# Kernel optimization log

Measured on AMD Instinct MI355X. Metric: run time of the kernel, lower is better.

Reference implementation:

```python
import jax, jax.numpy as jnp
import numpy as np

B, C, OC, H, W = 2, 64, 128, 96, 96
HD, DI, N, R, K = C // 2, C, 16, 2, 4  # VSSBlock: hidden=C/2, d_inner=2*hidden=C, d_state, dt_rank, 4 scan dirs
EPS = 1e-5


def _conv(x, w, b, pad, groups=1):
    y = jax.lax.conv_general_dilated(x, w, (1, 1), pad, feature_group_count=groups,
                                     dimension_numbers=('NCHW', 'OIHW', 'NCHW'))
    return y + b[None, :, None, None]


def _ln(x, w, b):
    m = x.mean(-1, keepdims=True)
    v = x.var(-1, keepdims=True)
    return (x - m) * jax.lax.rsqrt(v + EPS) * w + b


def _selective_scan(xs, dts, Bs, Cs, A, D):
    # xs, dts: (B,K,DI,L); Bs, Cs: (B,K,N,L); A: (K,DI,N); D: (K,DI)
    dts = jax.nn.softplus(dts)

    def step(h, inp):
        u_t, dt_t, B_t, C_t = inp
        dA = jnp.exp(dt_t[..., None] * A)                         # (B,K,DI,N)
        h = dA * h + (dt_t * u_t)[..., None] * B_t[:, :, None, :]
        return h, jnp.einsum('bkdn,bkn->bkd', h, C_t)

    seq = (jnp.moveaxis(xs, -1, 0), jnp.moveaxis(dts, -1, 0),
           jnp.moveaxis(Bs, -1, 0), jnp.moveaxis(Cs, -1, 0))
    h0 = jnp.zeros(xs.shape[:3] + (A.shape[-1],), xs.dtype)
    _, ys = jax.lax.scan(step, h0, seq)
    return jnp.moveaxis(ys, 0, -1) + D[None, :, :, None] * xs


def _vss_block(x, ln_w, ln_b, in_w, conv_w, conv_b, xproj_w, dtproj_w, dtproj_b,
               A_logs, Ds, on_w, on_b, out_w):
    # x: (B,H,W,HD); VMamba SS2D with 4-direction cross-scan + residual
    b, hh, ww, _ = x.shape
    L = hh * ww
    h = _ln(x, ln_w, ln_b)
    xz = h @ in_w                                   # (B,H,W,2*DI)
    xp, z = jnp.split(xz, 2, axis=-1)
    xc = jnp.transpose(xp, (0, 3, 1, 2))            # (B,DI,H,W)
    xc = jax.nn.silu(_conv(xc, conv_w, conv_b, ((1, 1), (1, 1)), groups=DI))
    x_flat = xc.reshape(b, DI, L)
    x_wh = jnp.transpose(xc, (0, 1, 3, 2)).reshape(b, DI, L)
    x2 = jnp.stack([x_flat, x_wh], axis=1)
    xs = jnp.concatenate([x2, jnp.flip(x2, -1)], axis=1)      # (B,4,DI,L)
    x_dbl = jnp.einsum('bkdl,kcd->bkcl', xs, xproj_w)
    dts, Bs, Cs = jnp.split(x_dbl, [R, R + N], axis=2)
    dts = jnp.einsum('bkrl,kdr->bkdl', dts, dtproj_w) + dtproj_b[None, :, :, None]
    A = -jnp.exp(A_logs)
    ys = _selective_scan(xs, dts, Bs, Cs, A, Ds)              # (B,4,DI,L)
    inv = jnp.flip(ys[:, 2:4], -1)
    unwh = lambda t: jnp.transpose(t.reshape(b, DI, ww, hh), (0, 1, 3, 2)).reshape(b, DI, L)
    y = ys[:, 0] + inv[:, 0] + unwh(ys[:, 1]) + unwh(inv[:, 1])
    y = jnp.transpose(y.reshape(b, DI, hh, ww), (0, 2, 3, 1))
    y = _ln(y, on_w, on_b) * jax.nn.silu(z)
    return x + y @ out_w


def _forward(x, ms_dw33_w, ms_dw33_b, ms_in_w, ms_in_b, ms_scale,
             vss_ln_w, vss_ln_b, vss_in_w, vss_conv_w, vss_conv_b, vss_xproj_w,
             vss_dtproj_w, vss_dtproj_b, vss_A_logs, vss_Ds, vss_on_w, vss_on_b, vss_out_w,
             ma_conv_w, ma_conv_b, adw_h_w, adw_h_b, adw_w_w, adw_w_b,
             pw_w, pw_b, bn_w, bn_b, bn_mean, bn_var):
    vss = (vss_ln_w, vss_ln_b, vss_in_w, vss_conv_w, vss_conv_b, vss_xproj_w,
           vss_dtproj_w, vss_dtproj_b, vss_A_logs, vss_Ds, vss_on_w, vss_on_b, vss_out_w)
    # --- MambaSplit (shared VSSBlock applied to both channel halves) ---
    xd = _conv(x, ms_dw33_w, ms_dw33_b, ((1, 1), (1, 1)), groups=C)
    x1, x2 = jnp.split(xd, 2, axis=1)

    def branch(xp):
        y = _vss_block(jnp.transpose(xp, (0, 2, 3, 1)), *vss)
        return ms_scale * xp + jnp.transpose(y, (0, 3, 1, 2))

    xm = jnp.concatenate([branch(x1), branch(x2)], axis=1)
    m = xm.mean((2, 3), keepdims=True)
    v = xm.var((2, 3), keepdims=True)
    xm = (xm - m) * jax.lax.rsqrt(v + EPS) * ms_in_w[None, :, None, None] + ms_in_b[None, :, None, None]
    xm = jax.nn.leaky_relu(xm, 0.01)
    # --- MaxAvg (global avg+max pool -> 3x3 conv on 1x1 map -> sigmoid gate) ---
    pooled = jnp.concatenate([x.mean((2, 3), keepdims=True), x.max((2, 3), keepdims=True)], axis=1)
    gate = jax.nn.sigmoid(_conv(pooled, ma_conv_w, ma_conv_b, ((1, 1), (1, 1))))
    xs_ = xm + gate * x
    # --- AxialDW ---
    xs_ = xs_ + _conv(xs_, adw_h_w, adw_h_b, ((1, 1), (0, 0)), groups=C) \
              + _conv(xs_, adw_w_w, adw_w_b, ((0, 0), (1, 1)), groups=C)
    # --- BN (eval) + ReLU, 1x1 conv, 2x2 maxpool ---
    skip = jax.nn.relu((xs_ - bn_mean[None, :, None, None]) * jax.lax.rsqrt(bn_var[None, :, None, None] + EPS)
                       * bn_w[None, :, None, None] + bn_b[None, :, None, None])
    out = _conv(skip, pw_w, pw_b, ((0, 0), (0, 0)))
    down = jax.lax.reduce_window(out, -jnp.inf, jax.lax.max, (1, 1, 2, 2), (1, 1, 2, 2), 'VALID')
    return down, skip


def setup_inputs() -> dict:
    key = jax.random.key(0)
    ks = jax.random.split(key, 16)
    r = lambda i, shape, s=0.02: jax.random.normal(ks[i], shape, jnp.float32) * s
    return {
        'x': jax.random.normal(ks[0], (B, C, H, W), jnp.float32),
        'ms_dw33_w': r(1, (C, 1, 3, 3), 0.1), 'ms_dw33_b': jnp.zeros(C),
        'ms_in_w': jnp.ones(C), 'ms_in_b': jnp.zeros(C),
        'ms_scale': jnp.ones((1,)),
        'vss_ln_w': jnp.ones(HD), 'vss_ln_b': jnp.zeros(HD),
        'vss_in_w': r(2, (HD, 2 * DI)),
        'vss_conv_w': r(3, (DI, 1, 3, 3), 0.1), 'vss_conv_b': jnp.zeros(DI),
        'vss_xproj_w': r(4, (K, R + 2 * N, DI)),
        'vss_dtproj_w': r(5, (K, DI, R), 0.1), 'vss_dtproj_b': r(6, (K, DI), 0.1),
        'vss_A_logs': jnp.tile(jnp.log(jnp.arange(1, N + 1, dtype=jnp.float32)), (K, DI, 1)),
        'vss_Ds': jnp.ones((K, DI)),
        'vss_on_w': jnp.ones(DI), 'vss_on_b': jnp.zeros(DI),
        'vss_out_w': r(7, (DI, HD)),
        'ma_conv_w': r(8, (C, 2 * C, 3, 3), 0.05), 'ma_conv_b': jnp.zeros(C),
        'adw_h_w': r(9, (C, 1, 3, 1), 0.1), 'adw_h_b': jnp.zeros(C),
        'adw_w_w': r(10, (C, 1, 1, 3), 0.1), 'adw_w_b': jnp.zeros(C),
        'pw_w': r(11, (OC, C, 1, 1)), 'pw_b': jnp.zeros(OC),
        'bn_w': jnp.ones(C), 'bn_b': jnp.zeros(C),
        'bn_mean': jnp.zeros(C), 'bn_var': jnp.ones(C),
    }


def reference(x, ms_dw33_w, ms_dw33_b, ms_in_w, ms_in_b, ms_scale,
              vss_ln_w, vss_ln_b, vss_in_w, vss_conv_w, vss_conv_b, vss_xproj_w,
              vss_dtproj_w, vss_dtproj_b, vss_A_logs, vss_Ds, vss_on_w, vss_on_b, vss_out_w,
              ma_conv_w, ma_conv_b, adw_h_w, adw_h_b, adw_w_w, adw_w_b,
              pw_w, pw_b, bn_w, bn_b, bn_mean, bn_var):
    return _forward(x, ms_dw33_w, ms_dw33_b, ms_in_w, ms_in_b, ms_scale,
                    vss_ln_w, vss_ln_b, vss_in_w, vss_conv_w, vss_conv_b, vss_xproj_w,
                    vss_dtproj_w, vss_dtproj_b, vss_A_logs, vss_Ds, vss_on_w, vss_on_b, vss_out_w,
                    ma_conv_w, ma_conv_b, adw_h_w, adw_h_b, adw_w_w, adw_w_b,
                    pw_w, pw_b, bn_w, bn_b, bn_mean, bn_var)
```

## Files before the change

kernel.cpp:

```cpp
#include <hip/hip_runtime.h>
#include <hip/hip_bf16.h>

typedef __hip_bfloat16 bf16;
#define DEV __device__ __forceinline__

constexpr int B_ = 2, C_ = 64, H_ = 96, W_ = 96, L_ = 9216;
constexpr int HD_ = 32, DI_ = 64, N_ = 16, K_ = 4, BB_ = 4;
constexpr int OC_ = 128;
constexpr int CH_ = 384, CL_ = 24;
constexpr int SEGN = 32, SEGC = 12;
constexpr int BROW = 20;
constexpr float EPSF = 1e-5f;
constexpr int DOWN_SZ = B_ * OC_ * 48 * 48;

typedef __attribute__((ext_vector_type(8))) short short8;
typedef __attribute__((ext_vector_type(4))) float f32x4;
typedef __attribute__((ext_vector_type(2))) float f32x2;

DEV float softplusf(float x) { return x > 15.f ? x : __logf(1.f + __expf(x)); }
DEV float b2f(bf16 v) { return __bfloat162float(v); }
DEV float lo16f(unsigned v) { return __uint_as_float(v << 16); }
DEV float hi16f(unsigned v) { return __uint_as_float(v & 0xffff0000u); }
DEV f32x2 pk2(unsigned w) { f32x2 r = {lo16f(w), hi16f(w)}; return r; }
DEV f32x2 lo2(f32x4 q) { f32x2 r = {q.x, q.y}; return r; }
DEV f32x2 hi2(f32x4 q) { f32x2 r = {q.z, q.w}; return r; }
DEV unsigned pkbf(float a, float b) {
  __hip_bfloat162 t;
  t.x = __float2bfloat16(a);
  t.y = __float2bfloat16(b);
  return *reinterpret_cast<unsigned*>(&t);
}
DEV void unpk8(uint4 a, float* v) {
  v[0] = lo16f(a.x); v[1] = hi16f(a.x); v[2] = lo16f(a.y); v[3] = hi16f(a.y);
  v[4] = lo16f(a.z); v[5] = hi16f(a.z); v[6] = lo16f(a.w); v[7] = hi16f(a.w);
}
DEV void unpk(uint4 a, uint4 b, float* v) {
  unpk8(a, v); unpk8(b, v + 8);
}

__constant__ float kLogN[16] = {
  0.0f, 0.69314718f, 1.09861229f, 1.38629436f, 1.60943791f, 1.79175947f,
  1.94591015f, 2.07944154f, 2.19722458f, 2.30258509f, 2.39789527f,
  2.48490665f, 2.56494936f, 2.63905733f, 2.70805020f, 2.77258872f};

DEV void pow_tree2(float e1, f32x2* ep) {
  float e2 = e1 * e1;
  ep[0].x = e1; ep[0].y = e2;
  f32x2 b2v = {e2, e2};
  ep[1] = ep[0] * b2v;
  float e4 = ep[1].y;
  f32x2 b4v = {e4, e4};
  ep[2] = ep[0] * b4v;
  ep[3] = ep[1] * b4v;
  float e8 = ep[3].y;
  f32x2 b8v = {e8, e8};
  ep[4] = ep[0] * b8v;
  ep[5] = ep[1] * b8v;
  ep[6] = ep[2] * b8v;
  ep[7] = ep[3] * b8v;
}

__global__ __launch_bounds__(256, 4) void k_front(
    const float* __restrict__ x, const float* __restrict__ dw33w,
    const float* __restrict__ dw33b, const float* __restrict__ lnw,
    const float* __restrict__ lnb, const float* __restrict__ inw,
    const float* __restrict__ xpw, const float* __restrict__ alog,
    float* __restrict__ xd, bf16* __restrict__ xzAh, bf16* __restrict__ xzBh,
    bf16* __restrict__ wh, float* __restrict__ aux) {
  int bb = blockIdx.y, t = threadIdx.x;
  int b = bb & 1, co = (bb >> 1) * HD_;
  int idx0 = blockIdx.x * 32;
  if (bb == 0) {
    int i = blockIdx.x * 256 + t;
    if (i < 144 * 64) {
      int n = i >> 6;
      wh[i] = __float2bfloat16(n < 136 ? xpw[i] : 0.f);
    }
    if (blockIdx.x == 0) {
      int kd = t;
      const float* al = alog + kd * N_;
      float a0 = al[0];
      bool lin = true;
#pragma unroll
      for (int n = 1; n < N_; n++) lin = lin && (fabsf(al[n] - a0 - kLogN[n]) < 3e-5f);
      aux[kd] = -__expf(a0);
      aux[256 + kd] = lin ? 1.f : 0.f;
#pragma unroll
      for (int n = 0; n < N_; n++) aux[512 + kd * N_ + n] = -__expf(al[n]);
    }
  }
  __shared__ float xds[32 * 36];
  __shared__ float meanA[32], rstdA[32];
  for (int i = t; i < 1024; i += 256) {
    int cl = i >> 5, ii = i & 31;
    int sp = idx0 + ii, wi = sp % 96, hi = sp / 96;
    int cg = b * C_ + co + cl;
    float acc = dw33b[co + cl];
#pragma unroll
    for (int dy = -1; dy <= 1; dy++) {
      int hh = hi + dy; if (hh < 0 || hh >= H_) continue;
#pragma unroll
      for (int dx = -1; dx <= 1; dx++) {
        int ww = wi + dx; if (ww < 0 || ww >= W_) continue;
        acc = fmaf(x[(size_t)cg * L_ + sp + dy * 96 + dx],
                   dw33w[(co + cl) * 9 + (dy + 1) * 3 + (dx + 1)], acc);
      }
    }
    xds[cl * 36 + ii] = acc;
    xd[(size_t)cg * L_ + sp] = acc;
  }
  __syncthreads();
  if (t < 32) {
    float s = 0.f, sq = 0.f;
#pragma unroll
    for (int c = 0; c < 32; c++) { float v = xds[c * 36 + t]; s += v; sq = fmaf(v, v, sq); }
    float mean = s * (1.f / HD_);
    float var = sq * (1.f / HD_) - mean * mean;
    meanA[t] = mean; rstdA[t] = rsqrtf(var + EPSF);
  }
  __syncthreads();
  for (int i = t; i < 1024; i += 256) {
    int c = i >> 5, idx = i & 31;
    float v = xds[c * 36 + idx];
    xds[c * 36 + idx] = (v - meanA[idx]) * rstdA[idx] * lnw[c] + lnb[c];
  }
  __syncthreads();
  int oc = t & 127, g = t >> 7;
  float acc[16];
#pragma unroll
  for (int j = 0; j < 16; j++) acc[j] = 0.f;
  for (int c = 0; c < 32; c++) {
    float wv = inw[c * 128 + oc];
    const float4* row = reinterpret_cast<const float4*>(&xds[c * 36 + g * 16]);
#pragma unroll
    for (int j4 = 0; j4 < 4; j4++) {
      float4 xv = row[j4];
      acc[j4 * 4 + 0] = fmaf(xv.x, wv, acc[j4 * 4 + 0]);
      acc[j4 * 4 + 1] = fmaf(xv.y, wv, acc[j4 * 4 + 1]);
      acc[j4 * 4 + 2] = fmaf(xv.z, wv, acc[j4 * 4 + 2]);
      acc[j4 * 4 + 3] = fmaf(xv.w, wv, acc[j4 * 4 + 3]);
    }
  }
  int occ = oc & 63;
  if (oc < 64) {
#pragma unroll
    for (int j = 0; j < 16; j++)
      xzAh[(size_t)(bb * L_ + idx0 + g * 16 + j) * 64 + occ] = __float2bfloat16(acc[j]);
  } else {
#pragma unroll
    for (int j = 0; j < 16; j++)
      xzBh[(size_t)(bb * L_ + idx0 + g * 16 + j) * 64 + occ] = __float2bfloat16(acc[j]);
  }
}

__global__ void k_dwsilu(const bf16* __restrict__ xzAh, const float* __restrict__ cw,
                         const float* __restrict__ cb, bf16* __restrict__ xch,
                         bf16* __restrict__ xcht) {
  int t = blockIdx.x * 256 + threadIdx.x;
  int dp = t & 31, rp = t >> 5;
  int bb = blockIdx.y;
  int d0 = dp * 2;
  int wi = rp % 96, hp = rp / 96;
  int hi0 = hp * 2;
  const unsigned* src = (const unsigned*)xzAh;
  float a00 = cb[d0], a01 = cb[d0 + 1];
  float a10 = a00, a11 = a01;
#pragma unroll
  for (int r4 = 0; r4 < 4; r4++) {
    int rr = hi0 - 1 + r4;
    if (rr < 0 || rr >= H_) continue;
#pragma unroll
    for (int c3 = 0; c3 < 3; c3++) {
      int cc = wi - 1 + c3;
      if (cc < 0 || cc >= W_) continue;
      unsigned v = src[(size_t)(bb * L_ + rr * 96 + cc) * 32 + dp];
      float vl = lo16f(v), vh = hi16f(v);
      if (r4 <= 2) {
        a00 = fmaf(vl, cw[d0 * 9 + r4 * 3 + c3], a00);
        a01 = fmaf(vh, cw[(d0 + 1) * 9 + r4 * 3 + c3], a01);
      }
      if (r4 >= 1) {
        a10 = fmaf(vl, cw[d0 * 9 + (r4 - 1) * 3 + c3], a10);
        a11 = fmaf(vh, cw[(d0 + 1) * 9 + (r4 - 1) * 3 + c3], a11);
      }
    }
  }
  a00 = a00 / (1.f + __expf(-a00));
  a01 = a01 / (1.f + __expf(-a01));
  a10 = a10 / (1.f + __expf(-a10));
  a11 = a11 / (1.f + __expf(-a11));
  unsigned o0 = pkbf(a00, a01), o1 = pkbf(a10, a11);
  int idx0 = hi0 * 96 + wi;
  ((unsigned*)xch)[((size_t)bb * L_ + idx0) * 32 + dp] = o0;
  ((unsigned*)xch)[((size_t)bb * L_ + idx0 + 96) * 32 + dp] = o1;
  int it0 = wi * 96 + hi0;
  ((unsigned*)xcht)[((size_t)bb * L_ + it0) * 32 + dp] = o0;
  ((unsigned*)xcht)[((size_t)bb * L_ + it0 + 1) * 32 + dp] = o1;
}

__global__ __launch_bounds__(256, 4) void k_xdbl_mfma(
    const bf16* __restrict__ xch, const bf16* __restrict__ wh,
    float* __restrict__ xdblB, float* __restrict__ xdblC) {
  int w = threadIdx.x >> 6, lane = threadIdx.x & 63;
  int bb = blockIdx.y;
  int mtile = blockIdx.x * 4 + w;
  int idx0 = mtile * 16;
  int m = lane & 15, quad = lane >> 4;
  const bf16* arow = xch + ((size_t)bb * L_ + idx0 + m) * 64 + quad * 8;
  short8 a0 = *reinterpret_cast<const short8*>(arow);
  short8 a1 = *reinterpret_cast<const short8*>(arow + 32);
  int ntb = blockIdx.z * 3;
#pragma unroll
  for (int it = 0; it < 3; it++) {
    int nt = ntb + it;
    int n = nt * 16 + m;
    const bf16* brow = wh + n * 64 + quad * 8;
    short8 b0 = *reinterpret_cast<const short8*>(brow);
    short8 b1 = *reinterpret_cast<const short8*>(brow + 32);
    f32x4 acc = {0.f, 0.f, 0.f, 0.f};
    acc = __builtin_amdgcn_mfma_f32_16x16x32_bf16(a0, b0, acc, 0, 0, 0);
    acc = __builtin_amdgcn_mfma_f32_16x16x32_bf16(a1, b1, acc, 0, 0, 0);
    if (n < 136) {
      int k4 = (n >= 102) ? 3 : (n >= 68) ? 2 : (n >= 34) ? 1 : 0;
      int c = n - k4 * 34;
#pragma unroll
      for (int i = 0; i < 4; i++) {
        int r = idx0 + quad * 4 + i;
        int hi2 = r / 96, wi2 = r - hi2 * 96;
        int tr = wi2 * 96 + hi2;
        int ls = (k4 == 0) ? r : (k4 == 1) ? tr : (k4 == 2) ? (L_ - 1 - r) : (L_ - 1 - tr);
        size_t row = (size_t)(bb * K_ + k4) * L_ + ls;
        if (c < 2)       xdblB[row * BROW + 16 + c] = acc[i];
        else if (c < 18) xdblB[row * BROW + (c - 2)] = acc[i];
        else             xdblC[row * 16 + (c - 18)] = acc[i];
      }
    }
  }
}

__global__ __launch_bounds__(256, 4) void k_scan1(
    const float* __restrict__ xdblB, const bf16* __restrict__ xch,
    const bf16* __restrict__ xcht, const float* __restrict__ dtw,
    const float* __restrict__ dtb, const float* __restrict__ aux,
    bf16* __restrict__ hbuf, float* __restrict__ ssum) {
  int w = threadIdx.x >> 6, d = threadIdx.x & 63;
  int bx = blockIdx.x;
  int chunk = bx * 4 + w, k = blockIdx.y, bb = blockIdx.z;
  const float* bB = xdblB + (size_t)(bb * K_ + k) * L_ * BROW;
  __shared__ __align__(16) float sB[96 * BROW];
  {
    const uint4* src = (const uint4*)(bB + (size_t)bx * 96 * BROW);
    uint4* dst = (uint4*)sB;
    for (int i = threadIdx.x; i < 480; i += 256) dst[i] = src[i];
  }
  __syncthreads();
  float w0 = dtw[(k * DI_ + d) * 2 + 0], w1 = dtw[(k * DI_ + d) * 2 + 1];
  float bia = dtb[k * DI_ + d];
  float A1 = aux[k * 64 + d];
  bool chain = (__ballot(aux[256 + k * 64 + d] > 0.5f) == ~0ull);
  const bf16* ub = ((k & 1) ? xcht : xch) + (size_t)bb * L_ * DI_;
  int ls0 = chunk * CL_;
  int uidx0 = (k & 2) ? (L_ - 1 - ls0) : ls0;
  int ustep = (k & 2) ? -1 : 1;
  float S = 0.f;
  size_t base = (size_t)((bb * K_ + k) * CH_ + chunk) * DI_ + d;
  if (chain) {
    float uv[CL_];
    const bf16* up = ub + (size_t)uidx0 * DI_ + d;
#pragma unroll
    for (int s = 0; s < CL_; s++) uv[s] = b2f(up[s * ustep * DI_]);
    f32x2 h2[8];
#pragma unroll
    for (int i = 0; i < 8; i++) { h2[i].x = 0.f; h2[i].y = 0.f; }
#pragma unroll
    for (int s = 0; s < CL_; s++) {
      const float* p = sB + (w * CL_ + s) * BROW;
      f32x4 q0 = *(const f32x4*)p;
      f32x4 q1 = *(const f32x4*)(p + 4);
      f32x4 q2 = *(const f32x4*)(p + 8);
      f32x4 q3 = *(const f32x4*)(p + 12);
      f32x2 tt = *(const f32x2*)(p + 16);
      float dt = softplusf(fmaf(tt.x, w0, fmaf(tt.y, w1, bia)));
      S += dt;
      float du = dt * uv[s];
      f32x2 du2 = {du, du};
      f32x2 ep2[8];
      pow_tree2(__expf(dt * A1), ep2);
      h2[0] = ep2[0] * h2[0] + du2 * lo2(q0);
      h2[1] = ep2[1] * h2[1] + du2 * hi2(q0);
      h2[2] = ep2[2] * h2[2] + du2 * lo2(q1);
      h2[3] = ep2[3] * h2[3] + du2 * hi2(q1);
      h2[4] = ep2[4] * h2[4] + du2 * lo2(q2);
      h2[5] = ep2[5] * h2[5] + du2 * hi2(q2);
      h2[6] = ep2[6] * h2[6] + du2 * lo2(q3);
      h2[7] = ep2[7] * h2[7] + du2 * hi2(q3);
    }
    uint4 o0, o1;
    o0.x = pkbf(h2[0].x, h2[0].y); o0.y = pkbf(h2[1].x, h2[1].y);
    o0.z = pkbf(h2[2].x, h2[2].y); o0.w = pkbf(h2[3].x, h2[3].y);
    o1.x = pkbf(h2[4].x, h2[4].y); o1.y = pkbf(h2[5].x, h2[5].y);
    o1.z = pkbf(h2[6].x, h2[6].y); o1.w = pkbf(h2[7].x, h2[7].y);
    *(uint4*)(hbuf + base * N_) = o0;
    *(uint4*)(hbuf + base * N_ + 8) = o1;
  } else {
    float h[N_];
#pragma unroll
    for (int n = 0; n < N_; n++) h[n] = 0.f;
    float A[N_];
#pragma unroll
    for (int n = 0; n < N_; n++) A[n] = aux[512 + (k * 64 + d) * N_ + n];
    for (int s = 0; s < CL_; s++) {
      const float* p = sB + (w * CL_ + s) * BROW;
      float u = b2f(ub[(size_t)(uidx0 + s * ustep) * DI_ + d]);
      float dt = softplusf(fmaf(p[16], w0, fmaf(p[17], w1, bia)));
      S += dt;
      float du = dt * u;
#pragma unroll
      for (int n = 0; n < N_; n++) h[n] = fmaf(__expf(dt * A[n]), h[n], du * p[n]);
    }
#pragma unroll
    for (int n = 0; n < N_; n++) hbuf[base * N_ + n] = __float2bfloat16(h[n]);
  }
  ssum[base] = S;
}

__global__ __launch_bounds__(256, 4) void k_scan2a(
    const float* __restrict__ aux, const float* __restrict__ ssum,
    bf16* __restrict__ hbuf, float* __restrict__ cumS,
    float* __restrict__ segH, float* __restrict__ segS) {
  int t = blockIdx.x * 256 + threadIdx.x;
  int n = t & 15, d = (t >> 4) & 63, kk = (t >> 10) & 3, bb = (t >> 12) & 3, seg = t >> 14;
  float A = aux[512 + (kk * 64 + d) * N_ + n];
  size_t row = (size_t)(bb * K_ + kk) * CH_ * DI_ + d;
  float hp = 0.f, Sc = 0.f;
#pragma unroll 4
  for (int j = 0; j < SEGC; j++) {
    int c = seg * SEGC + j;
    size_t sb = row + (size_t)c * DI_;
    float S = ssum[sb];
    float hl = b2f(hbuf[sb * N_ + n]);
    hbuf[sb * N_ + n] = __float2bfloat16(hp);
    if (n == 0) cumS[sb] = Sc;
    hp = fmaf(__expf(A * S), hp, hl);
    Sc += S;
  }
  size_t sbase = (size_t)(bb * K_ + kk) * SEGN + seg;
  segH[(sbase * DI_ + d) * N_ + n] = hp;
  if (n == 0) segS[sbase * DI_ + d] = Sc;
}

__global__ void k_scan2b(const float* __restrict__ aux, float* __restrict__ segH,
                         const float* __restrict__ segS) {
  int t = blockIdx.x * 256 + threadIdx.x;
  int n = t & 15, d = (t >> 4) & 63, kk = (t >> 10) & 3, bb = t >> 12;
  float A = aux[512 + (kk * 64 + d) * N_ + n];
  float hp = 0.f;
  for (int seg = 0; seg < SEGN; seg++) {
    size_t sbase = (size_t)(bb * K_ + kk) * SEGN + seg;
    size_t si = (sbase * DI_ + d) * N_ + n;
    float H = segH[si];
    float E = __expf(A * segS[sbase * DI_ + d]);
    segH[si] = hp;
    hp = fmaf(E, hp, H);
  }
}

__global__ __launch_bounds__(256, 4) void k_scan3(
    const float* __restrict__ xdblB, const float* __restrict__ xdblC,
    const bf16* __restrict__ xch, const bf16* __restrict__ xcht,
    const float* __restrict__ dtw, const float* __restrict__ dtb,
    const float* __restrict__ Dsw, const float* __restrict__ aux,
    const bf16* __restrict__ hbuf, const float* __restrict__ cumS,
    const float* __restrict__ segH, bf16* __restrict__ ydir) {
  int w = threadIdx.x >> 6, d = threadIdx.x & 63;
  int bx = blockIdx.x;
  int chunk = bx * 4 + w, k = blockIdx.y, bb = blockIdx.z;
  const float* bB = xdblB + (size_t)(bb * K_ + k) * L_ * BROW;
  const float* bC = xdblC + (size_t)(bb * K_ + k) * L_ * 16;
  __shared__ __align__(16) float sB[96 * BROW];
  __shared__ __align__(16) float sC[96 * 16];
  {
    const uint4* srcB = (const uint4*)(bB + (size_t)bx * 96 * BROW);
    uint4* dstB = (uint4*)sB;
    for (int i = threadIdx.x; i < 480; i += 256) dstB[i] = srcB[i];
    const uint4* srcC = (const uint4*)(bC + (size_t)bx * 96 * 16);
    uint4* dstC = (uint4*)sC;
    for (int i = threadIdx.x; i < 384; i += 256) dstC[i] = srcC[i];
  }
  __syncthreads();
  float w0 = dtw[(k * DI_ + d) * 2 + 0], w1 = dtw[(k * DI_ + d) * 2 + 1];
  float bia = dtb[k * DI_ + d];
  float Dk = Dsw[k * DI_ + d];
  float A1 = aux[k * 64 + d];
  bool chain = (__ballot(aux[256 + k * 64 + d] > 0.5f) == ~0ull);
  size_t base = (size_t)((bb * K_ + k) * CH_ + chunk) * DI_ + d;
  int seg = chunk / SEGC;
  size_t sbase = (size_t)(bb * K_ + k) * SEGN + seg;
  float Sc = cumS[base];
  const bf16* ub = ((k & 1) ? xcht : xch) + (size_t)bb * L_ * DI_;
  bf16* yb = ydir + (size_t)(bb * K_ + k) * L_ * DI_;
  int ls0 = chunk * CL_;
  int uidx0 = (k & 2) ? (L_ - 1 - ls0) : ls0;
  int ustep = (k & 2) ? -1 : 1;
  const bf16* hb = hbuf + base * N_;
  const float* Hin = segH + (sbase * DI_ + d) * N_;
  if (chain) {
    float uv[CL_];
    const bf16* up = ub + (size_t)uidx0 * DI_ + d;
#pragma unroll
    for (int s = 0; s < CL_; s++) uv[s] = b2f(up[s * ustep * DI_]);
    f32x2 h2[8];
    {
      uint4 qh0 = *(const uint4*)hb, qh1 = *(const uint4*)(hb + 8);
      h2[0] = pk2(qh0.x); h2[1] = pk2(qh0.y); h2[2] = pk2(qh0.z); h2[3] = pk2(qh0.w);
      h2[4] = pk2(qh1.x); h2[5] = pk2(qh1.y); h2[6] = pk2(qh1.z); h2[7] = pk2(qh1.w);
      f32x2 ep2[8];
      pow_tree2(__expf(A1 * Sc), ep2);
#pragma unroll
      for (int i = 0; i < 8; i++)
        h2[i] = ep2[i] * (*(const f32x2*)(Hin + 2 * i)) + h2[i];
    }
#pragma unroll
    for (int s = 0; s < CL_; s++) {
      int lr = w * CL_ + s;
      const float* p = sB + lr * BROW;
      const float* pc = sC + lr * 16;
      f32x4 q0 = *(const f32x4*)p;
      f32x4 q1 = *(const f32x4*)(p + 4);
      f32x4 q2 = *(const f32x4*)(p + 8);
      f32x4 q3 = *(const f32x4*)(p + 12);
      f32x2 tt = *(const f32x2*)(p + 16);
      f32x4 c0 = *(const f32x4*)pc;
      f32x4 c1 = *(const f32x4*)(pc + 4);
      f32x4 c2 = *(const f32x4*)(pc + 8);
      f32x4 c3 = *(const f32x4*)(pc + 12);
      float dt = softplusf(fmaf(tt.x, w0, fmaf(tt.y, w1, bia)));
      float du = dt * uv[s];
      f32x2 du2 = {du, du};
      f32x2 ep2[8];
      pow_tree2(__expf(dt * A1), ep2);
      f32x2 y2 = {0.f, 0.f};
      h2[0] = ep2[0] * h2[0] + du2 * lo2(q0);  y2 = h2[0] * lo2(c0) + y2;
      h2[1] = ep2[1] * h2[1] + du2 * hi2(q0);  y2 = h2[1] * hi2(c0) + y2;
      h2[2] = ep2[2] * h2[2] + du2 * lo2(q1);  y2 = h2[2] * lo2(c1) + y2;
      h2[3] = ep2[3] * h2[3] + du2 * hi2(q1);  y2 = h2[3] * hi2(c1) + y2;
      h2[4] = ep2[4] * h2[4] + du2 * lo2(q2);  y2 = h2[4] * lo2(c2) + y2;
      h2[5] = ep2[5] * h2[5] + du2 * hi2(q2);  y2 = h2[5] * hi2(c2) + y2;
      h2[6] = ep2[6] * h2[6] + du2 * lo2(q3);  y2 = h2[6] * lo2(c3) + y2;
      h2[7] = ep2[7] * h2[7] + du2 * hi2(q3);  y2 = h2[7] * hi2(c3) + y2;
      float y = fmaf(Dk, uv[s], y2.x + y2.y);
      yb[(size_t)(ls0 + s) * DI_ + d] = __float2bfloat16(y);
    }
  } else {
    float h[N_];
    {
      uint4 qh0 = *(const uint4*)hb, qh1 = *(const uint4*)(hb + 8);
      unpk(qh0, qh1, h);
#pragma unroll
      for (int n = 0; n < N_; n++) {
        float A = aux[512 + (k * 64 + d) * N_ + n];
        h[n] = fmaf(__expf(A * Sc), Hin[n], h[n]);
      }
    }
    float A[N_];
#pragma unroll
    for (int n = 0; n < N_; n++) A[n] = aux[512 + (k * 64 + d) * N_ + n];
    for (int s = 0; s < CL_; s++) {
      int lr = w * CL_ + s;
      const float* p = sB + lr * BROW;
      const float* pc = sC + lr * 16;
      float u = b2f(ub[(size_t)(uidx0 + s * ustep) * DI_ + d]);
      float dt = softplusf(fmaf(p[16], w0, fmaf(p[17], w1, bia)));
      float du = dt * u;
      float y = 0.f;
#pragma unroll
      for (int n = 0; n < N_; n++) {
        h[n] = fmaf(__expf(dt * A[n]), h[n], du * p[n]);
        y = fmaf(h[n], pc[n], y);
      }
      y = fmaf(Dk, u, y);
      yb[(size_t)(ls0 + s) * DI_ + d] = __float2bfloat16(y);
    }
  }
}

__global__ void k_combine(const bf16* __restrict__ ydir, const bf16* __restrict__ xzBh,
                          const float* __restrict__ xd, const float* __restrict__ onw,
                          const float* __restrict__ onb, const float* __restrict__ outw,
                          const float* __restrict__ mssc, float* __restrict__ xm) {
  int w = threadIdx.x >> 6, d = threadIdx.x & 63;
  int idxA = blockIdx.x * 8 + w * 2, bb = blockIdx.y;
  int idxB = idxA + 1;
  int b = bb & 1, co = (bb >> 1) * HD_;
  const bf16* yd = ydir + (size_t)bb * K_ * L_ * DI_;
  int hiA = idxA / 96, wiA = idxA - hiA * 96, ltA = wiA * 96 + hiA;
  int hiB = idxB / 96, wiB = idxB - hiB * 96, ltB = wiB * 96 + hiB;
  float yA = b2f(yd[((size_t)0 * L_ + idxA) * DI_ + d])
           + b2f(yd[((size_t)1 * L_ + ltA) * DI_ + d])
           + b2f(yd[((size_t)2 * L_ + (L_ - 1 - idxA)) * DI_ + d])
           + b2f(yd[((size_t)3 * L_ + (L_ - 1 - ltA)) * DI_ + d]);
  float yB = b2f(yd[((size_t)0 * L_ + idxB) * DI_ + d])
           + b2f(yd[((size_t)1 * L_ + ltB) * DI_ + d])
           + b2f(yd[((size_t)2 * L_ + (L_ - 1 - idxB)) * DI_ + d])
           + b2f(yd[((size_t)3 * L_ + (L_ - 1 - ltB)) * DI_ + d]);
  float sA = yA, qA = yA * yA, sB = yB, qB = yB * yB;
#pragma unroll
  for (int m = 1; m < 64; m <<= 1) {
    sA += __shfl_xor(sA, m, 64); qA += __shfl_xor(qA, m, 64);
    sB += __shfl_xor(sB, m, 64); qB += __shfl_xor(qB, m, 64);
  }
  float meanA = sA * (1.f / DI_);
  float rstdA = rsqrtf(qA * (1.f / DI_) - meanA * meanA + EPSF);
  float meanB = sB * (1.f / DI_);
  float rstdB = rsqrtf(qB * (1.f / DI_) - meanB * meanB + EPSF);
  float onwd = onw[d], onbd = onb[d];
  float ynA = (yA - meanA) * rstdA * onwd + onbd;
  float ynB = (yB - meanB) * rstdB * onwd + onbd;
  float zA = b2f(xzBh[(size_t)(bb * L_ + idxA) * 64 + d]);
  float zB = b2f(xzBh[(size_t)(bb * L_ + idxB) * 64 + d]);
  float gA = ynA * (zA / (1.f + __expf(-zA)));
  float gB = ynB * (zB / (1.f + __expf(-zB)));
  __shared__ __align__(16) float gs[8][DI_];
  gs[w * 2][d] = gA;
  gs[w * 2 + 1][d] = gB;
  __syncthreads();
  int dh = d & 31;
  int ddb = (d >= 32) ? 32 : 0;
  const float* ga = &gs[w * 2][ddb];
  const float* gb = &gs[w * 2 + 1][ddb];
  float accA = 0.f, accB = 0.f;
#pragma unroll
  for (int j = 0; j < 8; j++) {
    float4 va = *(const float4*)(ga + j * 4);
    float4 vb = *(const float4*)(gb + j * 4);
    int dd = ddb + j * 4;
    float w0 = outw[(dd + 0) * HD_ + dh];
    float w1 = outw[(dd + 1) * HD_ + dh];
    float w2 = outw[(dd + 2) * HD_ + dh];
    float w3 = outw[(dd + 3) * HD_ + dh];
    accA = fmaf(va.x, w0, accA); accB = fmaf(vb.x, w0, accB);
    accA = fmaf(va.y, w1, accA); accB = fmaf(vb.y, w1, accB);
    accA = fmaf(va.z, w2, accA); accB = fmaf(vb.z, w2, accB);
    accA = fmaf(va.w, w3, accA); accB = fmaf(vb.w, w3, accB);
  }
  accA += __shfl_xor(accA, 32, 64);
  accB += __shfl_xor(accB, 32, 64);
  if (d < HD_) {
    float sc = mssc[0] + 1.f;
    size_t xiA = (size_t)(b * C_ + co + d) * L_ + idxA;
    size_t xiB = (size_t)(b * C_ + co + d) * L_ + idxB;
    xm[xiA] = sc * xd[xiA] + accA;
    xm[xiB] = sc * xd[xiB] + accB;
  }
}

__global__ __launch_bounds__(1024) void k_stats(
    const float* __restrict__ xm, const float* __restrict__ x,
    float* __restrict__ inm, float* __restrict__ inr,
    float* __restrict__ xmean, float* __restrict__ xmax) {
  int bc = blockIdx.x, t = threadIdx.x;
  const float4* pm4 = (const float4*)(xm + (size_t)bc * L_);
  const float4* px4 = (const float4*)(x + (size_t)bc * L_);
  float s = 0.f, sq = 0.f, xs = 0.f, mx = -1e30f;
  for (int i = t; i < L_ / 4; i += 1024) {
    float4 v = pm4[i];
    s += (v.x + v.y) + (v.z + v.w);
    sq = fmaf(v.x, v.x, sq); sq = fmaf(v.y, v.y, sq);
    sq = fmaf(v.z, v.z, sq); sq = fmaf(v.w, v.w, sq);
    float4 xv = px4[i];
    xs += (xv.x + xv.y) + (xv.z + xv.w);
    mx = fmaxf(mx, fmaxf(fmaxf(xv.x, xv.y), fmaxf(xv.z, xv.w)));
  }
  __shared__ float red[64];
#pragma unroll
  for (int m = 1; m < 64; m <<= 1) {
    s += __shfl_xor(s, m, 64); sq += __shfl_xor(sq, m, 64);
    xs += __shfl_xor(xs, m, 64); mx = fmaxf(mx, __shfl_xor(mx, m, 64));
  }
  int wid = t >> 6;
  if ((t & 63) == 0) { red[wid] = s; red[16 + wid] = sq; red[32 + wid] = xs; red[48 + wid] = mx; }
  __syncthreads();
  if (t == 0) {
    s = 0.f; sq = 0.f; xs = 0.f; mx = -1e30f;
#pragma unroll
    for (int i = 0; i < 16; i++) {
      s += red[i]; sq += red[16 + i]; xs += red[32 + i]; mx = fmaxf(mx, red[48 + i]);
    }
    float mean = s * (1.f / L_);
    float var = sq * (1.f / L_) - mean * mean;
    inm[bc] = mean;
    inr[bc] = rsqrtf(var + EPSF);
    xmean[bc] = xs * (1.f / L_);
    xmax[bc] = mx;
  }
}

__global__ void k_axbn(const float* __restrict__ xm, const float* __restrict__ x,
                       const float* __restrict__ inm, const float* __restrict__ inr,
                       const float* __restrict__ msw, const float* __restrict__ msb,
                       const float* __restrict__ xmean, const float* __restrict__ xmax,
                       const float* __restrict__ maw, const float* __restrict__ mab,
                       const float* __restrict__ hw, const float* __restrict__ hb,
                       const float* __restrict__ wwt, const float* __restrict__ wb,
                       const float* __restrict__ bnw, const float* __restrict__ bnb,
                       const float* __restrict__ bnm, const float* __restrict__ bnv,
                       float* __restrict__ skipo) {
  constexpr int NEL = B_ * C_ * L_;
  int t0 = blockIdx.x * 512;
  int bc = t0 / L_, c = bc & 63, b = bc >> 6;
  __shared__ float gsh;
  __shared__ float sxs[704];
  if (threadIdx.x < 64) {
    int ic = threadIdx.x;
    float p = xmean[b * 64 + ic] * maw[(c * 128 + ic) * 9 + 4]
            + xmax[b * 64 + ic] * maw[(c * 128 + 64 + ic) * 9 + 4];
#pragma unroll
    for (int m = 1; m < 64; m <<= 1) p += __shfl_xor(p, m, 64);
    if (ic == 0) gsh = 1.f / (1.f + __expf(-(p + mab[c])));
  }
  __syncthreads();
  float gate = gsh, im = inm[bc], ir = inr[bc], mw = msw[c], mb = msb[c];
  for (int i = threadIdx.x; i < 704; i += 256) {
    int tt = t0 - 96 + i;
    tt = tt < 0 ? 0 : (tt >= NEL ? NEL - 1 : tt);
    float v = xm[tt];
    v = (v - im) * ir * mw + mb;
    v = v > 0.f ? v : 0.01f * v;
    sxs[i] = v + gate * x[tt];
  }
  __syncthreads();
  float hw0 = hw[c * 3], hw1 = hw[c * 3 + 1], hw2 = hw[c * 3 + 2];
  float ww0 = wwt[c * 3], ww1 = wwt[c * 3 + 1], ww2 = wwt[c * 3 + 2];
  float hbc = hb[c], wbc = wb[c];
  float bnr = rsqrtf(bnv[c] + EPSF) * bnw[c];
  float bnmc = bnm[c], bnbc = bnb[c];
#pragma unroll
  for (int e = 0; e < 2; e++) {
    int tid = e * 256 + threadIdx.x;
    int t = t0 + tid;
    int li = 96 + tid;
    int wi = t % W_, hi = (t / W_) % H_;
    float a = sxs[li];
    float hacc = hbc;
    if (hi > 0)      hacc = fmaf(sxs[li - 96], hw0, hacc);
    hacc = fmaf(a, hw1, hacc);
    if (hi < H_ - 1) hacc = fmaf(sxs[li + 96], hw2, hacc);
    float wacc = wbc;
    if (wi > 0)      wacc = fmaf(sxs[li - 1], ww0, wacc);
    wacc = fmaf(a, ww1, wacc);
    if (wi < W_ - 1) wacc = fmaf(sxs[li + 1], ww2, wacc);
    float v = a + hacc + wacc;
    float sv = (v - bnmc) * bnr + bnbc;
    skipo[t] = fmaxf(sv, 0.f);
  }
}

__global__ void k_pwpool(const float* __restrict__ skipo, const float* __restrict__ pww,
                         const float* __restrict__ pwb, float* __restrict__ down) {
  int h2 = blockIdx.x, b = blockIdx.y, t = threadIdx.x;
  int oc0 = blockIdx.z * 32;
  __shared__ __align__(8) float sk[64 * 192];
  for (int i = t; i < 64 * 192; i += 256) {
    int c = i / 192, rw = i % 192, r = rw / 96, wcol = rw % 96;
    sk[i] = skipo[((size_t)(b * C_ + c) * H_ + (2 * h2 + r)) * W_ + wcol];
  }
  __syncthreads();
  for (int o = t; o < 32 * 48; o += 256) {
    int oc = oc0 + o / 48, w2 = o % 48;
    float s0 = 0.f, s1 = 0.f, s2 = 0.f, s3 = 0.f;
#pragma unroll 8
    for (int c = 0; c < 64; c++) {
      float wv = pww[oc * 64 + c];
      const float2* sp = (const float2*)&sk[c * 192 + 2 * w2];
      float2 r0 = sp[0];
      float2 r1 = sp[48];
      s0 = fmaf(r0.x, wv, s0);
      s1 = fmaf(r0.y, wv, s1);
      s2 = fmaf(r1.x, wv, s2);
      s3 = fmaf(r1.y, wv, s3);
    }
    float v = fmaxf(fmaxf(s0, s1), fmaxf(s2, s3)) + pwb[oc];
    down[((size_t)(b * OC_ + oc) * 48 + h2) * 48 + w2] = v;
  }
}

extern "C" void kernel_launch(void* const* d_in, const int* in_sizes, int n_in,
                              void* d_out, int out_size, void* d_ws, size_t ws_size,
                              hipStream_t stream) {
  const float* x     = (const float*)d_in[0];
  const float* dw33w = (const float*)d_in[1];
  const float* dw33b = (const float*)d_in[2];
  const float* msw   = (const float*)d_in[3];
  const float* msb   = (const float*)d_in[4];
  const float* mssc  = (const float*)d_in[5];
  const float* lnw   = (const float*)d_in[6];
  const float* lnb   = (const float*)d_in[7];
  const float* inw   = (const float*)d_in[8];
  const float* cw    = (const float*)d_in[9];
  const float* cb    = (const float*)d_in[10];
  const float* xpw   = (const float*)d_in[11];
  const float* dtw   = (const float*)d_in[12];
  const float* dtb   = (const float*)d_in[13];
  const float* alog  = (const float*)d_in[14];
  const float* Dsw   = (const float*)d_in[15];
  const float* onw   = (const float*)d_in[16];
  const float* onb   = (const float*)d_in[17];
  const float* outw  = (const float*)d_in[18];
  const float* maw   = (const float*)d_in[19];
  const float* mab   = (const float*)d_in[20];
  const float* ahw   = (const float*)d_in[21];
  const float* ahb   = (const float*)d_in[22];
  const float* aww   = (const float*)d_in[23];
  const float* awb   = (const float*)d_in[24];
  const float* pww   = (const float*)d_in[25];
  const float* pwb   = (const float*)d_in[26];
  const float* bnw   = (const float*)d_in[27];
  const float* bnb   = (const float*)d_in[28];
  const float* bnm   = (const float*)d_in[29];
  const float* bnv   = (const float*)d_in[30];

  float* ws = (float*)d_ws;
  float* xd    = ws;
  float* hreg  = xd + 1179648;
  bf16*  hbuf  = (bf16*)hreg;
  bf16*  xzAh  = (bf16*)hreg;
  bf16*  xzBh  = (bf16*)(hreg + 1179648);
  float* xdblB = hreg + 1179648 + 1179648;
  float* xdblC = xdblB + 2949120;
  float* ssum  = xdblC + 2359296;
  bf16*  ydir  = (bf16*)(ssum + 393216);
  float* xmR   = ssum + 393216 + 4718592;
  bf16*  xch   = (bf16*)xmR;
  float* xm    = xmR;
  float* st    = xmR + 1179648;
  float* inm = st, *inr = st + 128, *xmean = st + 256, *xmaxv = st + 384;
  float* aux   = st + 512;
  bf16*  wh    = (bf16*)(aux + 4608);
  float* cumS  = aux + 4608 + 4608;
  float* segH  = cumS + 393216;
  float* segS  = segH + 524288;
  bf16*  xcht  = (bf16*)(segS + 32768);

  float* outp = (float*)d_out;
  float* down = outp;
  float* skipo = outp + DOWN_SZ;

  dim3 b256(256);
  int nEl = B_ * C_ * L_;

  k_front<<<dim3(L_ / 32, BB_), b256, 0, stream>>>(x, dw33w, dw33b, lnw, lnb, inw,
                                                   xpw, alog, xd, xzAh, xzBh, wh, aux);
  k_dwsilu<<<dim3(L_ / 2 * 32 / 256, BB_), b256, 0, stream>>>(xzAh, cw, cb, xch, xcht);
  k_xdbl_mfma<<<dim3(L_ / 64, BB_, 3), b256, 0, stream>>>(xch, wh, xdblB, xdblC);
  k_scan1<<<dim3(CH_ / 4, K_, BB_), b256, 0, stream>>>(xdblB, xch, xcht, dtw, dtb, aux, hbuf, ssum);
  k_scan2a<<<dim3(BB_ * K_ * SEGN * DI_ * N_ / 256), b256, 0, stream>>>(aux, ssum, hbuf, cumS, segH, segS);
  k_scan2b<<<dim3(BB_ * K_ * DI_ * N_ / 256), b256, 0, stream>>>(aux, segH, segS);
  k_scan3<<<dim3(CH_ / 4, K_, BB_), b256, 0, stream>>>(xdblB, xdblC, xch, xcht, dtw, dtb, Dsw,
                                                      aux, hbuf, cumS, segH, ydir);
  k_combine<<<dim3(L_ / 8, BB_), b256, 0, stream>>>(ydir, xzBh, xd, onw, onb, outw, mssc, xm);
  k_stats<<<dim3(B_ * C_), dim3(1024), 0, stream>>>(xm, x, inm, inr, xmean, xmaxv);
  k_axbn<<<dim3(nEl / 512), b256, 0, stream>>>(xm, x, inm, inr, msw, msb, xmean, xmaxv,
                                              maw, mab, ahw, ahb, aww, awb,
                                              bnw, bnb, bnm, bnv, skipo);
  k_pwpool<<<dim3(48, B_, 4), b256, 0, stream>>>(skipo, pww, pwb, down);
}
```

Measured before the change: 277.2 us.

## Fuse intra-block chunk prefix scan into scan1 and drop scan2a kernel

The per-block prefix combination of chunk states, previously done by the separate scan2a kernel, now runs inside scan1 through shared memory. The four warps' chunk states are combined in shared memory, and each block writes one segment summary, so there are 96 segments instead of 32. This removes a kernel launch and the global round trip through ssum and hbuf. In exchange the serial scan2b loop gets three times longer, the segH buffer is larger, and scan1 gains a sync plus extra exp work.

```diff
diff --git a/kernel.cpp b/kernel.cpp
--- a/kernel.cpp
+++ b/kernel.cpp
@@ -8,7 +8,7 @@
 constexpr int HD_ = 32, DI_ = 64, N_ = 16, K_ = 4, BB_ = 4;
 constexpr int OC_ = 128;
 constexpr int CH_ = 384, CL_ = 24;
-constexpr int SEGN = 32, SEGC = 12;
+constexpr int SEGN = 96, SEGC = 4;
 constexpr int BROW = 20;
 constexpr float EPSF = 1e-5f;
 constexpr int DOWN_SZ = B_ * OC_ * 48 * 48;
@@ -242,12 +242,15 @@
     const float* __restrict__ xdblB, const bf16* __restrict__ xch,
     const bf16* __restrict__ xcht, const float* __restrict__ dtw,
     const float* __restrict__ dtb, const float* __restrict__ aux,
-    bf16* __restrict__ hbuf, float* __restrict__ ssum) {
+    bf16* __restrict__ hbuf, float* __restrict__ cumS,
+    float* __restrict__ segH, float* __restrict__ segS) {
   int w = threadIdx.x >> 6, d = threadIdx.x & 63;
   int bx = blockIdx.x;
   int chunk = bx * 4 + w, k = blockIdx.y, bb = blockIdx.z;
   const float* bB = xdblB + (size_t)(bb * K_ + k) * L_ * BROW;
   __shared__ __align__(16) float sB[96 * BROW];
+  __shared__ float sHc[4][64][16];
+  __shared__ float sSc[4][64];
   {
     const uint4* src = (const uint4*)(bB + (size_t)bx * 96 * BROW);
     uint4* dst = (uint4*)sB;
@@ -263,7 +266,7 @@
   int uidx0 = (k & 2) ? (L_ - 1 - ls0) : ls0;
   int ustep = (k & 2) ? -1 : 1;
   float S = 0.f;
-  size_t base = (size_t)((bb * K_ + k) * CH_ + chunk) * DI_ + d;
+  float hout[16];
   if (chain) {
     float uv[CL_];
     const bf16* up = ub + (size_t)uidx0 * DI_ + d;
@@ -295,20 +298,15 @@
       h2[6] = ep2[6] * h2[6] + du2 * lo2(q3);
       h2[7] = ep2[7] * h2[7] + du2 * hi2(q3);
     }
-    uint4 o0, o1;
-    o0.x = pkbf(h2[0].x, h2[0].y); o0.y = pkbf(h2[1].x, h2[1].y);
-    o0.z = pkbf(h2[2].x, h2[2].y); o0.w = pkbf(h2[3].x, h2[3].y);
-    o1.x = pkbf(h2[4].x, h2[4].y); o1.y = pkbf(h2[5].x, h2[5].y);
-    o1.z = pkbf(h2[6].x, h2[6].y); o1.w = pkbf(h2[7].x, h2[7].y);
-    *(uint4*)(hbuf + base * N_) = o0;
-    *(uint4*)(hbuf + base * N_ + 8) = o1;
+#pragma unroll
+    for (int i = 0; i < 8; i++) { hout[2 * i] = h2[i].x; hout[2 * i + 1] = h2[i].y; }
   } else {
     float h[N_];
 #pragma unroll
     for (int n = 0; n < N_; n++) h[n] = 0.f;
-    float A[N_];
-#pragma unroll
-    for (int n = 0; n < N_; n++) A[n] = aux[512 + (k * 64 + d) * N_ + n];
+    float Ax[N_];
+#pragma unroll
+    for (int n = 0; n < N_; n++) Ax[n] = aux[512 + (k * 64 + d) * N_ + n];
     for (int s = 0; s < CL_; s++) {
       const float* p = sB + (w * CL_ + s) * BROW;
       float u = b2f(ub[(size_t)(uidx0 + s * ustep) * DI_ + d]);
@@ -316,37 +314,46 @@
       S += dt;
       float du = dt * u;
 #pragma unroll
-      for (int n = 0; n < N_; n++) h[n] = fmaf(__expf(dt * A[n]), h[n], du * p[n]);
-    }
-#pragma unroll
-    for (int n = 0; n < N_; n++) hbuf[base * N_ + n] = __float2bfloat16(h[n]);
-  }
-  ssum[base] = S;
-}
-
-__global__ __launch_bounds__(256, 4) void k_scan2a(
-    const float* __restrict__ aux, const float* __restrict__ ssum,
-    bf16* __restrict__ hbuf, float* __restrict__ cumS,
-    float* __restrict__ segH, float* __restrict__ segS) {
-  int t = blockIdx.x * 256 + threadIdx.x;
-  int n = t & 15, d = (t >> 4) & 63, kk = (t >> 10) & 3, bb = (t >> 12) & 3, seg = t >> 14;
-  float A = aux[512 + (kk * 64 + d) * N_ + n];
-  size_t row = (size_t)(bb * K_ + kk) * CH_ * DI_ + d;
-  float hp = 0.f, Sc = 0.f;
-#pragma unroll 4
-  for (int j = 0; j < SEGC; j++) {
-    int c = seg * SEGC + j;
-    size_t sb = row + (size_t)c * DI_;
-    float S = ssum[sb];
-    float hl = b2f(hbuf[sb * N_ + n]);
-    hbuf[sb * N_ + n] = __float2bfloat16(hp);
-    if (n == 0) cumS[sb] = Sc;
-    hp = fmaf(__expf(A * S), hp, hl);
-    Sc += S;
-  }
-  size_t sbase = (size_t)(bb * K_ + kk) * SEGN + seg;
-  segH[(sbase * DI_ + d) * N_ + n] = hp;
-  if (n == 0) segS[sbase * DI_ + d] = Sc;
+      for (int n = 0; n < N_; n++) h[n] = fmaf(__expf(dt * Ax[n]), h[n], du * p[n]);
+    }
+#pragma unroll
+    for (int n = 0; n < N_; n++) hout[n] = h[n];
+  }
+  sSc[w][d] = S;
+#pragma unroll
+  for (int n = 0; n < N_; n++) sHc[w][d][n] = hout[n];
+  __syncthreads();
+  float A[N_];
+#pragma unroll
+  for (int n = 0; n < N_; n++) A[n] = aux[512 + (k * 64 + d) * N_ + n];
+  float hp[N_];
+#pragma unroll
+  for (int n = 0; n < N_; n++) hp[n] = 0.f;
+  float Sc = 0.f;
+  for (int w2 = 0; w2 < w; w2++) {
+    float Sw = sSc[w2][d];
+#pragma unroll
+    for (int n = 0; n < N_; n++)
+      hp[n] = fmaf(__expf(A[n] * Sw), hp[n], sHc[w2][d][n]);
+    Sc += Sw;
+  }
+  size_t base = (size_t)((bb * K_ + k) * CH_ + chunk) * DI_ + d;
+  cumS[base] = Sc;
+  uint4 o0, o1;
+  o0.x = pkbf(hp[0], hp[1]);   o0.y = pkbf(hp[2], hp[3]);
+  o0.z = pkbf(hp[4], hp[5]);   o0.w = pkbf(hp[6], hp[7]);
+  o1.x = pkbf(hp[8], hp[9]);   o1.y = pkbf(hp[10], hp[11]);
+  o1.z = pkbf(hp[12], hp[13]); o1.w = pkbf(hp[14], hp[15]);
+  *(uint4*)(hbuf + base * N_) = o0;
+  *(uint4*)(hbuf + base * N_ + 8) = o1;
+  if (w == 3) {
+    size_t sb2 = (size_t)(bb * K_ + k) * SEGN + bx;
+    float* sh = segH + (sb2 * DI_ + d) * N_;
+#pragma unroll
+    for (int n = 0; n < N_; n++)
+      sh[n] = fmaf(__expf(A[n] * S), hp[n], hout[n]);
+    segS[sb2 * DI_ + d] = Sc + S;
+  }
 }
 
 __global__ void k_scan2b(const float* __restrict__ aux, float* __restrict__ segH,
@@ -724,12 +731,11 @@
   float* hreg  = xd + 1179648;
   bf16*  hbuf  = (bf16*)hreg;
   bf16*  xzAh  = (bf16*)hreg;
-  bf16*  xzBh  = (bf16*)(hreg + 1179648);
-  float* xdblB = hreg + 1179648 + 1179648;
+  bf16*  xzBh  = (bf16*)(hreg + 3145728);
+  float* xdblB = hreg + 3145728 + 1179648;
   float* xdblC = xdblB + 2949120;
-  float* ssum  = xdblC + 2359296;
-  bf16*  ydir  = (bf16*)(ssum + 393216);
-  float* xmR   = ssum + 393216 + 4718592;
+  bf16*  ydir  = (bf16*)(xdblC + 2359296);
+  float* xmR   = xdblC + 2359296 + 4718592;
   bf16*  xch   = (bf16*)xmR;
   float* xm    = xmR;
   float* st    = xmR + 1179648;
@@ -738,8 +744,8 @@
   bf16*  wh    = (bf16*)(aux + 4608);
   float* cumS  = aux + 4608 + 4608;
   float* segH  = cumS + 393216;
-  float* segS  = segH + 524288;
-  bf16*  xcht  = (bf16*)(segS + 32768);
+  float* segS  = segH + 1572864;
+  bf16*  xcht  = (bf16*)(segS + 98304);
 
   float* outp = (float*)d_out;
   float* down = outp;
@@ -752,8 +758,8 @@
                                                    xpw, alog, xd, xzAh, xzBh, wh, aux);
   k_dwsilu<<<dim3(L_ / 2 * 32 / 256, BB_), b256, 0, stream>>>(xzAh, cw, cb, xch, xcht);
   k_xdbl_mfma<<<dim3(L_ / 64, BB_, 3), b256, 0, stream>>>(xch, wh, xdblB, xdblC);
-  k_scan1<<<dim3(CH_ / 4, K_, BB_), b256, 0, stream>>>(xdblB, xch, xcht, dtw, dtb, aux, hbuf, ssum);
-  k_scan2a<<<dim3(BB_ * K_ * SEGN * DI_ * N_ / 256), b256, 0, stream>>>(aux, ssum, hbuf, cumS, segH, segS);
+  k_scan1<<<dim3(CH_ / 4, K_, BB_), b256, 0, stream>>>(xdblB, xch, xcht, dtw, dtb, aux,
+                                                      hbuf, cumS, segH, segS);
   k_scan2b<<<dim3(BB_ * K_ * DI_ * N_ / 256), b256, 0, stream>>>(aux, segH, segS);
   k_scan3<<<dim3(CH_ / 4, K_, BB_), b256, 0, stream>>>(xdblB, xdblC, xch, xcht, dtw, dtb, Dsw,
                                                       aux, hbuf, cumS, segH, ydir);
```

Measured after the change: 289.9 us. +4.6%, slower.
